# Optimization experiments

Hardware: AMD Instinct MI355X
Metric: run time of the kernel (lower is better)

Reference implementation:

```python
import jax, jax.numpy as jnp
import numpy as np


def setup_inputs() -> dict:
    key = jax.random.key(0)
    ks = jax.random.split(key, 6)
    B, S, C, D, E, EMB = 512, 512, 32, 512, 8, 32
    x = jax.random.normal(ks[0], (B, S, C), dtype=jnp.float32)
    Wp = jax.random.normal(ks[1], (C, D), dtype=jnp.float32) / np.sqrt(C)
    bp = jnp.zeros((D,), dtype=jnp.float32)
    emb = jax.random.normal(ks[2], (E, EMB), dtype=jnp.float32)
    Wg = jax.random.normal(ks[3], (D + EMB,), dtype=jnp.float32) / np.sqrt(D + EMB)
    bg = jnp.zeros((1,), dtype=jnp.float32)
    We = jax.random.normal(ks[4], (E, S, D), dtype=jnp.float32) / np.sqrt(S)
    return {"x": x, "Wp": Wp, "bp": bp, "emb": emb, "Wg": Wg, "bg": bg,
            "We": We, "k": 2}


def reference(x, Wp, bp, emb, Wg, bg, We, k):
    # x: [B, S, C]  (batch, seq_len, enc_in)
    B, S, C = x.shape
    E = We.shape[0]
    # RevIN 'subtract_median' normalization along the sequence dim
    xn = x - jnp.median(x, axis=1, keepdims=True)  # [B, S, C]
    # gating context from the last timestep, projected to d_model
    ctx = xn[:, -1, :] @ Wp + bp                    # [B, D]
    # condition gate on expert-identity embeddings: concat([ctx, emb_e])
    feat = jnp.concatenate(
        [jnp.broadcast_to(ctx[:, None, :], (B, E, ctx.shape[-1])),
         jnp.broadcast_to(emb[None, :, :], (B, E, emb.shape[-1]))],
        axis=-1)                                    # [B, E, D+EMB]
    clean_logits = feat @ Wg + bg[0]                # [B, E]
    # top-k gating (eval path: no noise), softmax over the k selected logits
    top_v, top_i = jax.lax.top_k(clean_logits, k)   # [B, k]
    top_g = jax.nn.softmax(top_v, axis=-1)          # [B, k]
    gates = jnp.zeros((B, E), dtype=x.dtype)
    gates = gates.at[jnp.arange(B)[:, None], top_i].set(top_g)  # sparse [B, E]
    # per-expert linear along seq: expert e maps [S, C] -> [D, C]
    expert_out = jnp.einsum('bsv,esd->ebdv', xn, We)  # [E, B, D, C]
    # weighted scatter-combine (equals SparseDispatcher.combine since
    # gates are zero outside the top-k set)
    combined = jnp.einsum('be,ebdv->bdv', gates, expert_out)  # [B, D, C]
    return combined
```

## Files before the change

### kernel.cpp

```cpp
#include <hip/hip_runtime.h>

typedef unsigned int u32;
typedef unsigned short u16;
typedef float f32x4 __attribute__((ext_vector_type(4)));
typedef short s16x8 __attribute__((ext_vector_type(8)));

#define Bn 512
#define Sn 512
#define Cn 32
#define Dn 512

__device__ __forceinline__ u32 f2bf(float f) {
  u32 u = __float_as_uint(f);
  return (u + 0x7FFFu + ((u >> 16) & 1u)) >> 16;
}
__device__ __forceinline__ float bfval(u32 bits) { return __uint_as_float(bits << 16); }
__device__ __forceinline__ float keyToFloat(u32 k) {
  u32 u = (k & 0x80000000u) ? (k ^ 0x80000000u) : ~k;
  return __uint_as_float(u);
}
__device__ __forceinline__ void gl2lds16(const void* g, void* l) {
  __builtin_amdgcn_global_load_lds(
      (const __attribute__((address_space(1))) u32*)g,
      (__attribute__((address_space(3))) u32*)l, 16, 0, 0);
}

__global__ __launch_bounds__(256) void k_pw(const float* __restrict__ x,
                                            const float* __restrict__ emb,
                                            const float* __restrict__ Wg,
                                            const float* __restrict__ We,
                                            float* __restrict__ med,
                                            u16* __restrict__ xbf,
                                            u16* __restrict__ WmT,
                                            float* __restrict__ cpart) {
  __shared__ float buf[512][17];
  __shared__ float ed[8];
  int blk = blockIdx.x;
  int t = threadIdx.x;

  if (blk < 1024) {
    int b = blk >> 1, half = blk & 1;
    int vbase = half * 16;
    int w = t >> 6, l = t & 63;
    const float4* xb4 = (const float4*)(x + (size_t)b * Sn * Cn);
    float4 f[8];
#pragma unroll
    for (int i = 0; i < 8; ++i)
      f[i] = xb4[((t >> 2) + i * 64) * 8 + half * 4 + (t & 3)];
#pragma unroll
    for (int i = 0; i < 8; ++i) {
      int s = (t >> 2) + i * 64, c0 = (t & 3) * 4;
      buf[s][c0 + 0] = f[i].x; buf[s][c0 + 1] = f[i].y;
      buf[s][c0 + 2] = f[i].z; buf[s][c0 + 3] = f[i].w;
    }
    __syncthreads();
    u32 K[4][8];
#pragma unroll
    for (int cc = 0; cc < 4; ++cc)
#pragma unroll
      for (int j = 0; j < 8; ++j) {
        u32 u = __float_as_uint(buf[j * 64 + l][w * 4 + cc]);
        K[cc][j] = (u >> 31) ? ~u : (u | 0x80000000u);
      }
    {
      int vl = t >> 4, sb = (t & 15) * 32;
      u16* orow = xbf + ((size_t)(b * 32 + vbase + vl)) * Sn;
#pragma unroll
      for (int cq = 0; cq < 4; ++cq) {
        int cp = (cq + (t & 15)) & 3;
        u32 pk[4];
#pragma unroll
        for (int jj = 0; jj < 4; ++jj) {
          u32 lo = f2bf(buf[sb + cp * 8 + jj * 2][vl]);
          u32 hi = f2bf(buf[sb + cp * 8 + jj * 2 + 1][vl]);
          pk[jj] = lo | (hi << 16);
        }
        *(uint4*)(orow + sb + cp * 8) = *(uint4*)pk;
      }
    }
    int base = b * 32 + vbase + w * 4;
#pragma unroll
    for (int cc = 0; cc < 4; ++cc) {
      u32 a1 = 0;
#pragma unroll
      for (int bit = 31; bit >= 0; --bit) {
        u32 cand = a1 | (1u << bit);
        int c = 0;
#pragma unroll
        for (int j = 0; j < 8; ++j) c += __popcll(__ballot(K[cc][j] < cand));
        if (c <= 255) a1 = cand;
      }
      int cle = 0;
#pragma unroll
      for (int j = 0; j < 8; ++j) cle += __popcll(__ballot(K[cc][j] <= a1));
      u32 a2;
      if (cle >= 257) {
        a2 = a1;
      } else {
        u32 mn = 0xFFFFFFFFu;
#pragma unroll
        for (int j = 0; j < 8; ++j) {
          u32 k2 = K[cc][j];
          if (k2 > a1 && k2 < mn) mn = k2;
        }
        mn = min(mn, (u32)__shfl_xor((int)mn, 1, 64));
        mn = min(mn, (u32)__shfl_xor((int)mn, 2, 64));
        mn = min(mn, (u32)__shfl_xor((int)mn, 4, 64));
        mn = min(mn, (u32)__shfl_xor((int)mn, 8, 64));
        mn = min(mn, (u32)__shfl_xor((int)mn, 16, 64));
        mn = min(mn, (u32)__shfl_xor((int)mn, 32, 64));
        a2 = mn;
      }
      if (l == 0) med[base + cc] = 0.5f * (keyToFloat(a1) + keyToFloat(a2));
    }
  } else {
    float (*tile)[65] = (float(*)[65])&buf[0][0];
    int bi2 = blk - 1024;
    int si = bi2 & 7, sb = si * 64, db = (bi2 >> 3) * 64;
    if (t < 8) {
      float s = 0.f;
#pragma unroll
      for (int j = 0; j < 32; ++j) s += emb[t * 32 + j] * Wg[Dn + j];
      ed[t] = s;
    }
    __syncthreads();
    int i1 = 0;
#pragma unroll
    for (int e = 1; e < 8; ++e) if (ed[e] > ed[i1]) i1 = e;
    int i2 = (i1 == 0) ? 1 : 0;
#pragma unroll
    for (int e = 0; e < 8; ++e) if (e != i1 && ed[e] > ed[i2]) i2 = e;
    float aa = ed[i1], bb = ed[i2];
    float m = fmaxf(aa, bb);
    float ea = __expf(aa - m), eb = __expf(bb - m);
    float inv = 1.f / (ea + eb);
    float g1 = ea * inv, g2 = eb * inv;
    const float* W1 = We + (size_t)i1 * Sn * Dn;
    const float* W2 = We + (size_t)i2 * Sn * Dn;
#pragma unroll
    for (int i = 0; i < 16; ++i) {
      int idx = t + i * 256;
      int sl = idx >> 6, dl = idx & 63;
      int g = (sb + sl) * Dn + db + dl;
      tile[sl][dl] = g1 * W1[g] + g2 * W2[g];
    }
    __syncthreads();
#pragma unroll
    for (int i = 0; i < 16; ++i) {
      int idx = t + i * 256;
      int dl = idx >> 6, sl = idx & 63;
      WmT[(size_t)(db + dl) * Sn + sb + sl] = (u16)f2bf(tile[sl][dl]);
    }
    {
      int dl = t >> 2, part = t & 3;
      float s = 0.f;
#pragma unroll
      for (int j = 0; j < 16; ++j)
        s += bfval(f2bf(tile[part * 16 + j][dl]));
      s += __shfl_xor(s, 1, 64);
      s += __shfl_xor(s, 2, 64);
      if (part == 0) cpart[si * 512 + db + dl] = s;
    }
  }
}

__global__ __launch_bounds__(256) void k_gemm(const u16* __restrict__ WmT,
                                              const u16* __restrict__ xbf,
                                              const float* __restrict__ med,
                                              const float* __restrict__ cpart,
                                              float* __restrict__ out) {
  __shared__ __align__(16) u16 As[128 * 64];
  __shared__ __align__(16) u16 Bs[128 * 64];
  __shared__ float csum[512];
  int bi = blockIdx.x;
  int mb = bi & 3, nb = bi >> 2;
  int t = threadIdx.x, w = t >> 6, l = t & 63;
  int mh = (w & 1) * 64, nh = (w >> 1) * 64;
  int lane16 = l & 15, q = l >> 4;
#pragma unroll
  for (int d = t; d < 512; d += 256) {
    float s = 0.f;
#pragma unroll
    for (int j = 0; j < 8; ++j) s += cpart[j * 512 + d];
    csum[d] = s;
  }
  f32x4 acc[4][4] = {};
  int r0 = t >> 3, c = t & 7;
  const u16* Ab = WmT + (size_t)(mb * 128) * Sn;
  const u16* Bb = xbf + (size_t)(nb * 128) * Sn;
#pragma unroll 1
  for (int ch = 0; ch < 8; ++ch) {
    int k0 = ch * 64;
#pragma unroll
    for (int i = 0; i < 4; ++i) {
      int r = r0 + i * 32;
      int gc = c ^ (r & 7);
      gl2lds16(Ab + (size_t)r * Sn + k0 + gc * 8, (char*)As + t * 16 + i * 4096);
      gl2lds16(Bb + (size_t)r * Sn + k0 + gc * 8, (char*)Bs + t * 16 + i * 4096);
    }
    __syncthreads();
#pragma unroll
    for (int kk = 0; kk < 2; ++kk) {
      s16x8 af[4], bf[4];
#pragma unroll
      for (int mt = 0; mt < 4; ++mt) {
        int m = mh + mt * 16 + lane16;
        int cs = (kk * 4 + q) ^ (m & 7);
        af[mt] = *(const s16x8*)(As + m * 64 + cs * 8);
      }
#pragma unroll
      for (int nt = 0; nt < 4; ++nt) {
        int n = nh + nt * 16 + lane16;
        int cs = (kk * 4 + q) ^ (n & 7);
        bf[nt] = *(const s16x8*)(Bs + n * 64 + cs * 8);
      }
#pragma unroll
      for (int mt = 0; mt < 4; ++mt)
#pragma unroll
        for (int nt = 0; nt < 4; ++nt)
          acc[mt][nt] = __builtin_amdgcn_mfma_f32_16x16x32_bf16(af[mt], bf[nt], acc[mt][nt], 0, 0, 0);
    }
    __syncthreads();
  }
#pragma unroll
  for (int nt = 0; nt < 4; ++nt) {
    int n = nb * 128 + nh + nt * 16 + lane16;
    int b = n >> 5, v = n & 31;
    float mv = med[n];
    float* obase = out + (size_t)b * (Dn * Cn) + v;
#pragma unroll
    for (int mt = 0; mt < 4; ++mt) {
      int d0 = mb * 128 + mh + mt * 16 + q * 4;
#pragma unroll
      for (int r = 0; r < 4; ++r)
        obase[(size_t)(d0 + r) * Cn] = acc[mt][nt][r] - mv * csum[d0 + r];
    }
  }
}

extern "C" void kernel_launch(void* const* d_in, const int* in_sizes, int n_in,
                              void* d_out, int out_size, void* d_ws, size_t ws_size,
                              hipStream_t stream) {
  const float* x   = (const float*)d_in[0];
  const float* emb = (const float*)d_in[3];
  const float* Wg  = (const float*)d_in[4];
  const float* We  = (const float*)d_in[6];
  float* out = (float*)d_out;
  char* ws = (char*)d_ws;
  float* med   = (float*)(ws);
  float* cpart = (float*)(ws + 65536);
  u16*   WmT   = (u16*)(ws + 65536 + 16384);
  u16*   xbf   = (u16*)(ws + 65536 + 16384 + 524288);

  hipLaunchKernelGGL(k_pw,   dim3(1088), dim3(256), 0, stream,
                     x, emb, Wg, We, med, xbf, WmT, cpart);
  hipLaunchKernelGGL(k_gemm, dim3(512),  dim3(256), 0, stream,
                     WmT, xbf, med, cpart, out);
}
```

Baseline: 141.3 us.

## Triple-buffer GEMM loads with 512-thread 128x256 tiles and interleave median bit searches

The GEMM kernel now uses 512 threads per block and a 128x256 output tile, with a three-stage LDS ring buffer. Global-to-LDS loads for chunk ch+2 are issued while chunk ch is computed, and the code syncs with explicit vmcnt waits plus raw barriers instead of __syncthreads. Block indices are remapped so that blocks sharing an XCD reuse B rows. The median bisection loop is restructured to interleave the four channels per bit, which exposes independent ballots. In exchange the kernel uses more LDS (about 144KB) and launches only 256 blocks, and correctness depends on the hand-set waitcnt values.

```diff
diff --git a/kernel.cpp b/kernel.cpp
--- a/kernel.cpp
+++ b/kernel.cpp
@@ -79,17 +79,22 @@
       }
     }
     int base = b * 32 + vbase + w * 4;
+    u32 a1v[4] = {0u, 0u, 0u, 0u};
+#pragma unroll 1
+    for (int bit = 31; bit >= 0; --bit) {
+      u32 msk = 1u << bit;
+#pragma unroll
+      for (int cc = 0; cc < 4; ++cc) {
+        u32 cand = a1v[cc] | msk;
+        int c = 0;
+#pragma unroll
+        for (int j = 0; j < 8; ++j) c += __popcll(__ballot(K[cc][j] < cand));
+        if (c <= 255) a1v[cc] = cand;
+      }
+    }
 #pragma unroll
     for (int cc = 0; cc < 4; ++cc) {
-      u32 a1 = 0;
-#pragma unroll
-      for (int bit = 31; bit >= 0; --bit) {
-        u32 cand = a1 | (1u << bit);
-        int c = 0;
-#pragma unroll
-        for (int j = 0; j < 8; ++j) c += __popcll(__ballot(K[cc][j] < cand));
-        if (c <= 255) a1 = cand;
-      }
+      u32 a1 = a1v[cc];
       int cle = 0;
 #pragma unroll
       for (int j = 0; j < 8; ++j) cle += __popcll(__ballot(K[cc][j] <= a1));
@@ -164,67 +169,94 @@
   }
 }
 
-__global__ __launch_bounds__(256) void k_gemm(const u16* __restrict__ WmT,
+__global__ __launch_bounds__(512) void k_gemm(const u16* __restrict__ WmT,
                                               const u16* __restrict__ xbf,
                                               const float* __restrict__ med,
                                               const float* __restrict__ cpart,
                                               float* __restrict__ out) {
-  __shared__ __align__(16) u16 As[128 * 64];
-  __shared__ __align__(16) u16 Bs[128 * 64];
+  __shared__ __align__(16) u16 As[3][128 * 64];
+  __shared__ __align__(16) u16 Bs[3][256 * 64];
   __shared__ float csum[512];
-  int bi = blockIdx.x;
-  int mb = bi & 3, nb = bi >> 2;
+  int g = blockIdx.x;
+  int xcd = g & 7, slot = g >> 3;
+  int nb = xcd * 8 + (slot >> 2);
+  int mb = slot & 3;
   int t = threadIdx.x, w = t >> 6, l = t & 63;
   int mh = (w & 1) * 64, nh = (w >> 1) * 64;
   int lane16 = l & 15, q = l >> 4;
-#pragma unroll
-  for (int d = t; d < 512; d += 256) {
+  {
     float s = 0.f;
 #pragma unroll
-    for (int j = 0; j < 8; ++j) s += cpart[j * 512 + d];
-    csum[d] = s;
-  }
+    for (int j = 0; j < 8; ++j) s += cpart[j * 512 + t];
+    csum[t] = s;
+  }
+  const u16* Ab = WmT + (size_t)(mb * 128) * Sn;
+  const u16* Bb = xbf + (size_t)(nb * 256) * Sn;
+  int r0 = t >> 3, c0 = t & 7;
+
+#define STAGE(ch, bf_) do {                                                      \
+    int k0 = (ch) * 64;                                                          \
+    _Pragma("unroll")                                                            \
+    for (int i = 0; i < 2; ++i) {                                                \
+      int r = r0 + i * 64;                                                       \
+      int gc = c0 ^ (r & 7);                                                     \
+      gl2lds16(Ab + (size_t)r * Sn + k0 + gc * 8,                                \
+               (char*)As[bf_] + t * 16 + i * 8192);                              \
+    }                                                                            \
+    _Pragma("unroll")                                                            \
+    for (int i = 0; i < 4; ++i) {                                                \
+      int r = r0 + i * 64;                                                       \
+      int gc = c0 ^ (r & 7);                                                     \
+      gl2lds16(Bb + (size_t)r * Sn + k0 + gc * 8,                                \
+               (char*)Bs[bf_] + t * 16 + i * 8192);                              \
+    }                                                                            \
+  } while (0)
+
   f32x4 acc[4][4] = {};
-  int r0 = t >> 3, c = t & 7;
-  const u16* Ab = WmT + (size_t)(mb * 128) * Sn;
-  const u16* Bb = xbf + (size_t)(nb * 128) * Sn;
-#pragma unroll 1
+  STAGE(0, 0);
+  STAGE(1, 1);
+  asm volatile("s_waitcnt lgkmcnt(0)" ::: "memory");
+  asm volatile("s_waitcnt vmcnt(6)" ::: "memory");
+  __builtin_amdgcn_s_barrier();
+  asm volatile("" ::: "memory");
+#pragma unroll
   for (int ch = 0; ch < 8; ++ch) {
-    int k0 = ch * 64;
-#pragma unroll
-    for (int i = 0; i < 4; ++i) {
-      int r = r0 + i * 32;
-      int gc = c ^ (r & 7);
-      gl2lds16(Ab + (size_t)r * Sn + k0 + gc * 8, (char*)As + t * 16 + i * 4096);
-      gl2lds16(Bb + (size_t)r * Sn + k0 + gc * 8, (char*)Bs + t * 16 + i * 4096);
-    }
-    __syncthreads();
+    int cur = ch % 3;
+    if (ch < 6) STAGE(ch + 2, (ch + 2) % 3);
+    const u16* Ac = As[cur];
+    const u16* Bc = Bs[cur];
 #pragma unroll
     for (int kk = 0; kk < 2; ++kk) {
-      s16x8 af[4], bf[4];
+      s16x8 af[4], bfr[4];
 #pragma unroll
       for (int mt = 0; mt < 4; ++mt) {
         int m = mh + mt * 16 + lane16;
         int cs = (kk * 4 + q) ^ (m & 7);
-        af[mt] = *(const s16x8*)(As + m * 64 + cs * 8);
+        af[mt] = *(const s16x8*)(Ac + m * 64 + cs * 8);
       }
 #pragma unroll
       for (int nt = 0; nt < 4; ++nt) {
         int n = nh + nt * 16 + lane16;
         int cs = (kk * 4 + q) ^ (n & 7);
-        bf[nt] = *(const s16x8*)(Bs + n * 64 + cs * 8);
+        bfr[nt] = *(const s16x8*)(Bc + n * 64 + cs * 8);
       }
 #pragma unroll
       for (int mt = 0; mt < 4; ++mt)
 #pragma unroll
         for (int nt = 0; nt < 4; ++nt)
-          acc[mt][nt] = __builtin_amdgcn_mfma_f32_16x16x32_bf16(af[mt], bf[nt], acc[mt][nt], 0, 0, 0);
-    }
-    __syncthreads();
-  }
+          acc[mt][nt] = __builtin_amdgcn_mfma_f32_16x16x32_bf16(af[mt], bfr[nt], acc[mt][nt], 0, 0, 0);
+    }
+    if (ch < 7) {
+      if (ch < 6) { asm volatile("s_waitcnt vmcnt(6)" ::: "memory"); }
+      else        { asm volatile("s_waitcnt vmcnt(0)" ::: "memory"); }
+      __builtin_amdgcn_s_barrier();
+      asm volatile("" ::: "memory");
+    }
+  }
+#undef STAGE
 #pragma unroll
   for (int nt = 0; nt < 4; ++nt) {
-    int n = nb * 128 + nh + nt * 16 + lane16;
+    int n = nb * 256 + nh + nt * 16 + lane16;
     int b = n >> 5, v = n & 31;
     float mv = med[n];
     float* obase = out + (size_t)b * (Dn * Cn) + v;
@@ -254,6 +286,6 @@
 
   hipLaunchKernelGGL(k_pw,   dim3(1088), dim3(256), 0, stream,
                      x, emb, Wg, We, med, xbf, WmT, cpart);
-  hipLaunchKernelGGL(k_gemm, dim3(512),  dim3(256), 0, stream,
+  hipLaunchKernelGGL(k_gemm, dim3(256),  dim3(512), 0, stream,
                      WmT, xbf, med, cpart, out);
 }
```

Result: faster. 136.2 us (median of 2 runs) (-3.7%).

## Double-buffer GEMM LDS loads, remap blocks per XCD, interleave median bisection

Applied to the files above, without the earlier changes.

The GEMM kernel now double-buffers its A/B tiles in LDS. The next K-chunk's global-to-LDS loads are issued while MFMAs run on the current chunk, using explicit vmcnt waits, barriers and raised wave priority. Block indices in both kernels are remapped so consecutive blocks on the same XCD share batch rows or B tiles for L2 locality. The median bit-bisection now interleaves its four columns per bit, so the independent ballots can overlap latency. The column-sum reduction moves after the main loop. These changes add LDS usage, which may lower occupancy, and rely on hand-tuned waitcnt values.

```diff
diff --git a/kernel.cpp b/kernel.cpp
--- a/kernel.cpp
+++ b/kernel.cpp
@@ -39,7 +39,9 @@
   int t = threadIdx.x;
 
   if (blk < 1024) {
-    int b = blk >> 1, half = blk & 1;
+    int xcd = blk & 7, sub = blk >> 3;
+    int b = xcd * 64 + (sub & 63);
+    int half = sub >> 6;
     int vbase = half * 16;
     int w = t >> 6, l = t & 63;
     const float4* xb4 = (const float4*)(x + (size_t)b * Sn * Cn);
@@ -79,17 +81,22 @@
       }
     }
     int base = b * 32 + vbase + w * 4;
+    u32 a1v[4] = {0u, 0u, 0u, 0u};
+#pragma unroll 1
+    for (int bit = 31; bit >= 0; --bit) {
+      u32 msk = 1u << bit;
+#pragma unroll
+      for (int cc = 0; cc < 4; ++cc) {
+        u32 cand = a1v[cc] | msk;
+        int c = 0;
+#pragma unroll
+        for (int j = 0; j < 8; ++j) c += __popcll(__ballot(K[cc][j] < cand));
+        if (c <= 255) a1v[cc] = cand;
+      }
+    }
 #pragma unroll
     for (int cc = 0; cc < 4; ++cc) {
-      u32 a1 = 0;
-#pragma unroll
-      for (int bit = 31; bit >= 0; --bit) {
-        u32 cand = a1 | (1u << bit);
-        int c = 0;
-#pragma unroll
-        for (int j = 0; j < 8; ++j) c += __popcll(__ballot(K[cc][j] < cand));
-        if (c <= 255) a1 = cand;
-      }
+      u32 a1 = a1v[cc];
       int cle = 0;
 #pragma unroll
       for (int j = 0; j < 8; ++j) cle += __popcll(__ballot(K[cc][j] <= a1));
@@ -169,59 +176,84 @@
                                               const float* __restrict__ med,
                                               const float* __restrict__ cpart,
                                               float* __restrict__ out) {
-  __shared__ __align__(16) u16 As[128 * 64];
-  __shared__ __align__(16) u16 Bs[128 * 64];
+  __shared__ __align__(16) u16 As[2][128 * 64];
+  __shared__ __align__(16) u16 Bs[2][128 * 64];
   __shared__ float csum[512];
   int bi = blockIdx.x;
-  int mb = bi & 3, nb = bi >> 2;
+  int xcd = bi & 7, sub = bi >> 3;
+  int mb = sub & 3, nb = xcd * 16 + (sub >> 2);
   int t = threadIdx.x, w = t >> 6, l = t & 63;
   int mh = (w & 1) * 64, nh = (w >> 1) * 64;
   int lane16 = l & 15, q = l >> 4;
-#pragma unroll
-  for (int d = t; d < 512; d += 256) {
-    float s = 0.f;
-#pragma unroll
-    for (int j = 0; j < 8; ++j) s += cpart[j * 512 + d];
-    csum[d] = s;
-  }
-  f32x4 acc[4][4] = {};
   int r0 = t >> 3, c = t & 7;
   const u16* Ab = WmT + (size_t)(mb * 128) * Sn;
   const u16* Bb = xbf + (size_t)(nb * 128) * Sn;
-#pragma unroll 1
+
+#define STAGE(ch, bf_) do {                                                      \
+    int k0 = (ch) * 64;                                                          \
+    _Pragma("unroll")                                                            \
+    for (int i = 0; i < 4; ++i) {                                                \
+      int r = r0 + i * 32;                                                       \
+      int gc = c ^ (r & 7);                                                      \
+      gl2lds16(Ab + (size_t)r * Sn + k0 + gc * 8,                                \
+               (char*)As[bf_] + t * 16 + i * 4096);                              \
+      gl2lds16(Bb + (size_t)r * Sn + k0 + gc * 8,                                \
+               (char*)Bs[bf_] + t * 16 + i * 4096);                              \
+    }                                                                            \
+  } while (0)
+
+  f32x4 acc[4][4] = {};
+  STAGE(0, 0);
+  STAGE(1, 1);
+  asm volatile("s_waitcnt vmcnt(8)" ::: "memory");
+  __builtin_amdgcn_s_barrier();
+#pragma unroll
   for (int ch = 0; ch < 8; ++ch) {
-    int k0 = ch * 64;
-#pragma unroll
-    for (int i = 0; i < 4; ++i) {
-      int r = r0 + i * 32;
-      int gc = c ^ (r & 7);
-      gl2lds16(Ab + (size_t)r * Sn + k0 + gc * 8, (char*)As + t * 16 + i * 4096);
-      gl2lds16(Bb + (size_t)r * Sn + k0 + gc * 8, (char*)Bs + t * 16 + i * 4096);
-    }
-    __syncthreads();
+    const u16* Ac = As[ch & 1];
+    const u16* Bc = Bs[ch & 1];
+    s16x8 af[2][4], bq[2][4];
 #pragma unroll
     for (int kk = 0; kk < 2; ++kk) {
-      s16x8 af[4], bf[4];
 #pragma unroll
       for (int mt = 0; mt < 4; ++mt) {
         int m = mh + mt * 16 + lane16;
         int cs = (kk * 4 + q) ^ (m & 7);
-        af[mt] = *(const s16x8*)(As + m * 64 + cs * 8);
+        af[kk][mt] = *(const s16x8*)(Ac + m * 64 + cs * 8);
       }
 #pragma unroll
       for (int nt = 0; nt < 4; ++nt) {
         int n = nh + nt * 16 + lane16;
         int cs = (kk * 4 + q) ^ (n & 7);
-        bf[nt] = *(const s16x8*)(Bs + n * 64 + cs * 8);
-      }
+        bq[kk][nt] = *(const s16x8*)(Bc + n * 64 + cs * 8);
+      }
+    }
+    asm volatile("s_waitcnt lgkmcnt(0)" ::: "memory");
+    __builtin_amdgcn_s_barrier();
+    if (ch < 6) STAGE(ch + 2, ch & 1);
+    __builtin_amdgcn_s_setprio(1);
+#pragma unroll
+    for (int kk = 0; kk < 2; ++kk)
 #pragma unroll
       for (int mt = 0; mt < 4; ++mt)
 #pragma unroll
         for (int nt = 0; nt < 4; ++nt)
-          acc[mt][nt] = __builtin_amdgcn_mfma_f32_16x16x32_bf16(af[mt], bf[nt], acc[mt][nt], 0, 0, 0);
-    }
-    __syncthreads();
-  }
+          acc[mt][nt] = __builtin_amdgcn_mfma_f32_16x16x32_bf16(af[kk][mt], bq[kk][nt], acc[mt][nt], 0, 0, 0);
+    __builtin_amdgcn_s_setprio(0);
+    if (ch < 7) {
+      if (ch < 6) { asm volatile("s_waitcnt vmcnt(8)" ::: "memory"); }
+      else        { asm volatile("s_waitcnt vmcnt(0)" ::: "memory"); }
+      __builtin_amdgcn_s_barrier();
+    }
+  }
+#undef STAGE
+#pragma unroll
+  for (int d = t; d < 512; d += 256) {
+    float s = 0.f;
+#pragma unroll
+    for (int j = 0; j < 8; ++j) s += cpart[j * 512 + d];
+    csum[d] = s;
+  }
+  __syncthreads();
 #pragma unroll
   for (int nt = 0; nt < 4; ++nt) {
     int n = nb * 128 + nh + nt * 16 + lane16;
```

New measurement: 136.3 us. 3.6% less time.
